# Optimization experiments

Hardware: AMD Instinct MI355X
Metric: run time of the kernel (lower is better)

The kernel has to match this reference:

```python
import jax, jax.numpy as jnp
import numpy as np

B, S, D = 8, 1024, 1024
H, DK, DV = 16, 64, 64
LN_EPS = 1e-5
NEG = -1.0e9


def setup_inputs() -> dict:
    key = jax.random.key(0)
    k1, k2, k3, k4, k5, k6, k7 = jax.random.split(key, 7)
    sc = 0.02
    input_Q = jax.random.normal(k1, (B, S, D), dtype=jnp.float32)
    input_K = jax.random.normal(k2, (B, S, D), dtype=jnp.float32)
    input_V = jax.random.normal(k3, (B, S, D), dtype=jnp.float32)
    # causal mask: True = masked (as in torch masked_fill_)
    attn_mask = jnp.broadcast_to(jnp.triu(jnp.ones((S, S), dtype=bool), k=1), (B, S, S))
    Wq = jax.random.normal(k4, (D, H * DK), dtype=jnp.float32) * sc
    Wk = jax.random.normal(k5, (D, H * DK), dtype=jnp.float32) * sc
    Wv = jax.random.normal(k6, (D, H * DV), dtype=jnp.float32) * sc
    Wfc = jax.random.normal(k7, (H * DV, D), dtype=jnp.float32) * sc
    return {"input_Q": input_Q, "input_K": input_K, "input_V": input_V,
            "attn_mask": attn_mask, "Wq": Wq, "Wk": Wk, "Wv": Wv, "Wfc": Wfc}


def _layernorm(x):
    mu = jnp.mean(x, axis=-1, keepdims=True)
    var = jnp.var(x, axis=-1, keepdims=True)
    return (x - mu) * jax.lax.rsqrt(var + LN_EPS)  # gamma=1, beta=0 (fresh nn.LayerNorm)


def reference(input_Q, input_K, input_V, attn_mask, Wq, Wk, Wv, Wfc):
    residual = input_Q
    # project and split heads: [B,S,H*dk] -> [B,H,S,dk]
    Q = (input_Q @ Wq).reshape(B, S, H, DK).transpose(0, 2, 1, 3)
    K = (input_K @ Wk).reshape(B, S, H, DK).transpose(0, 2, 1, 3)
    V = (input_V @ Wv).reshape(B, S, H, DV).transpose(0, 2, 1, 3)
    scores = jnp.einsum('bhqd,bhkd->bhqk', Q, K) / np.sqrt(DK).astype(np.float32)
    scores = jnp.where(attn_mask[:, None, :, :], NEG, scores)
    attn = jax.nn.softmax(scores, axis=-1)            # [B,H,S,S]
    context = jnp.einsum('bhqk,bhkd->bhqd', attn, V)  # [B,H,S,dv]
    context = context.transpose(0, 2, 1, 3).reshape(B, S, H * DV)
    out = _layernorm(residual + context @ Wfc)        # [B,S,D]
    return out, attn
```

## Files before the change

kernel.cpp:

```cpp
#include <hip/hip_runtime.h>
#include <hip/hip_bf16.h>

#define BB 8
#define SS 1024
#define DD 1024
#define HH 16
#define DKK 64
#define MM (BB*SS)
#define OUT_ELEMS ((size_t)BB*SS*DD)
#define ATTN_ELEMS ((size_t)BB*HH*SS*SS)

using short8 = __attribute__((ext_vector_type(8))) short;
using f32x4  = __attribute__((ext_vector_type(4))) float;

__device__ __forceinline__ ushort f2b(float f) {
    unsigned u = __float_as_uint(f);
    u = u + 0x7fffu + ((u >> 16) & 1u);
    return (ushort)(u >> 16);
}

__global__ __launch_bounds__(256) void transpose_w(
    const float* __restrict__ w0, const float* __restrict__ w1,
    const float* __restrict__ w2, const float* __restrict__ w3,
    ushort* __restrict__ t0, ushort* __restrict__ t1,
    ushort* __restrict__ t2, ushort* __restrict__ t3)
{
    const float* W; ushort* T;
    switch (blockIdx.z) {
        case 0: W = w0; T = t0; break;
        case 1: W = w1; T = t1; break;
        case 2: W = w2; T = t2; break;
        default: W = w3; T = t3; break;
    }
    __shared__ float tile[64 * 65];
    const int k0 = blockIdx.x * 64, n0 = blockIdx.y * 64;
    const int t = threadIdx.x;
#pragma unroll
    for (int i = 0; i < 16; i++) {
        int idx = i * 256 + t;
        int r = idx >> 6, c = idx & 63;
        tile[r * 65 + c] = W[(size_t)(k0 + r) * DD + n0 + c];
    }
    __syncthreads();
#pragma unroll
    for (int i = 0; i < 16; i++) {
        int idx = i * 256 + t;
        int nr = idx >> 6, kc = idx & 63;
        T[(size_t)(n0 + nr) * DD + k0 + kc] = f2b(tile[kc * 65 + nr]);
    }
}

template <int MODE>
__global__ __launch_bounds__(256) void gemm_bt(
    const float* __restrict__ A, const ushort* __restrict__ Bt,
    void* __restrict__ Cout)
{
    constexpr int K = 1024;
    const int t = threadIdx.x;
    const int wg = blockIdx.x;
    const int l  = (wg & 7) * 64 + (wg >> 3);
    const int n0 = (l & 7) * 128, m0 = (l >> 3) * 128;
    const int lane = t & 63, w = t >> 6;
    const int li = lane & 15, quad = lane >> 4;
    const int wm = w >> 1, wn = w & 1;

    __shared__ ushort As[128 * 40];

    f32x4 acc[4][4];
    const f32x4 zf = {0.f, 0.f, 0.f, 0.f};
#pragma unroll
    for (int mf = 0; mf < 4; mf++)
#pragma unroll
        for (int nf = 0; nf < 4; nf++) acc[mf][nf] = zf;

    for (int kk = 0; kk < K; kk += 32) {
        __syncthreads();
#pragma unroll
        for (int i = 0; i < 4; i++) {
            int row = (t >> 3) + i * 32;
            float4 a4 = *(const float4*)&A[(size_t)(m0 + row) * K + kk + (t & 7) * 4];
            ushort4 u4 = make_ushort4(f2b(a4.x), f2b(a4.y), f2b(a4.z), f2b(a4.w));
            *(ushort4*)&As[row * 40 + (t & 7) * 4] = u4;
        }
        __syncthreads();

        short8 af[4], bf[4];
#pragma unroll
        for (int mf = 0; mf < 4; mf++)
            af[mf] = *(const short8*)&As[(wm * 64 + mf * 16 + li) * 40 + quad * 8];
#pragma unroll
        for (int nf = 0; nf < 4; nf++)
            bf[nf] = *(const short8*)&Bt[(size_t)(n0 + wn * 64 + nf * 16 + li) * K + kk + quad * 8];
#pragma unroll
        for (int mf = 0; mf < 4; mf++)
#pragma unroll
            for (int nf = 0; nf < 4; nf++)
                acc[mf][nf] = __builtin_amdgcn_mfma_f32_16x16x32_bf16(af[mf], bf[nf], acc[mf][nf], 0, 0, 0);
    }

#pragma unroll
    for (int mf = 0; mf < 4; mf++)
#pragma unroll
        for (int nf = 0; nf < 4; nf++)
#pragma unroll
            for (int r = 0; r < 4; r++) {
                int m = m0 + wm * 64 + mf * 16 + quad * 4 + r;
                int n = n0 + wn * 64 + nf * 16 + li;
                float v = acc[mf][nf][r];
                if (MODE == 0) {
                    int b = m >> 10, s = m & 1023, h = n >> 6, d = n & 63;
                    ((ushort*)Cout)[((size_t)(b * HH + h) * SS + s) * 64 + d] = f2b(v);
                } else if (MODE == 1) {
                    int b = m >> 10, s = m & 1023, h = n >> 6, d = n & 63;
                    ((ushort*)Cout)[((size_t)(b * HH + h) * 64 + d) * SS + s] = f2b(v);
                } else {
                    ((float*)Cout)[(size_t)m * 1024 + n] = v;
                }
            }
}

__global__ __launch_bounds__(256) void attn_pv(
    const ushort* __restrict__ Qp, const ushort* __restrict__ Kp,
    const ushort* __restrict__ VpT, float* __restrict__ Invs,
    float* __restrict__ Ctx)
{
    const int pr = blockIdx.x;
    const int h  = blockIdx.y;
    const int b  = blockIdx.z;
    const int bh = b * HH + h;
    const int t = threadIdx.x;
    const int w = t >> 6, lane = t & 63;
    const int li = lane & 15, quad = lane >> 4;

    const ushort* Qh = Qp  + (size_t)bh * SS * 64;
    const ushort* Kh = Kp  + (size_t)bh * SS * 64;
    const ushort* Vt = VpT + (size_t)bh * 64 * SS;

    __shared__ ushort Ps[4][16 * 32];
    ushort* myP = Ps[w];
    const f32x4 zf = {0.f, 0.f, 0.f, 0.f};

    for (int sel = 0; sel < 2; sel++) {
        const int qt = sel ? (15 - pr) : pr;
        const int qbase = qt * 64 + w * 16;

        short8 aq0 = *(const short8*)&Qh[(size_t)(qbase + li) * 64 + quad * 8];
        short8 aq1 = *(const short8*)&Qh[(size_t)(qbase + li) * 64 + 32 + quad * 8];

        float lsum[4] = {0.f, 0.f, 0.f, 0.f};
        f32x4 cacc[4];
#pragma unroll
        for (int vf = 0; vf < 4; vf++) cacc[vf] = zf;

        const int nch = (qt + 1) * 2;

        for (int c = 0; c < nch; c++) {
            const int kb = c * 32;
#pragma unroll
            for (int half = 0; half < 2; half++) {
                const int col = kb + half * 16 + li;
                short8 bk0 = *(const short8*)&Kh[(size_t)col * 64 + quad * 8];
                short8 bk1 = *(const short8*)&Kh[(size_t)col * 64 + 32 + quad * 8];
                f32x4 s = __builtin_amdgcn_mfma_f32_16x16x32_bf16(aq0, bk0, zf, 0, 0, 0);
                s = __builtin_amdgcn_mfma_f32_16x16x32_bf16(aq1, bk1, s, 0, 0, 0);
#pragma unroll
                for (int r = 0; r < 4; r++) {
                    const int row = qbase + quad * 4 + r;
                    float p = (col <= row) ? __expf(s[r] * 0.125f) : 0.f;
                    lsum[r] += p;
                    myP[(quad * 4 + r) * 32 + half * 16 + li] = f2b(p);
                }
            }
            asm volatile("" ::: "memory");
            short8 ap = *(const short8*)&myP[li * 32 + quad * 8];
#pragma unroll
            for (int vf = 0; vf < 4; vf++) {
                short8 bv = *(const short8*)&Vt[(size_t)(vf * 16 + li) * SS + kb + quad * 8];
                cacc[vf] = __builtin_amdgcn_mfma_f32_16x16x32_bf16(ap, bv, cacc[vf], 0, 0, 0);
            }
            asm volatile("" ::: "memory");
        }

#pragma unroll
        for (int r = 0; r < 4; r++) {
            float v = lsum[r];
            v += __shfl_xor(v, 1, 64);
            v += __shfl_xor(v, 2, 64);
            v += __shfl_xor(v, 4, 64);
            v += __shfl_xor(v, 8, 64);
            lsum[r] = 1.f / v;
        }
        if (li == 0) {
#pragma unroll
            for (int r = 0; r < 4; r++)
                Invs[(size_t)bh * SS + qbase + quad * 4 + r] = lsum[r];
        }

#pragma unroll
        for (int vf = 0; vf < 4; vf++)
#pragma unroll
            for (int r = 0; r < 4; r++) {
                const int s_idx = qbase + quad * 4 + r;
                Ctx[((size_t)b * SS + s_idx) * DD + h * 64 + vf * 16 + li] = cacc[vf][r] * lsum[r];
            }
    }
}

__global__ __launch_bounds__(256) void attn_write(
    const ushort* __restrict__ Qp, const ushort* __restrict__ Kp,
    const float* __restrict__ Invs, float* __restrict__ attn)
{
    const int qt = blockIdx.x >> 1;
    const int ch = blockIdx.x & 1;
    const int h  = blockIdx.y;
    const int b  = blockIdx.z;
    const int bh = b * HH + h;
    const int t = threadIdx.x;
    const int w = t >> 6, lane = t & 63;
    const int li = lane & 15, quad = lane >> 4;
    const int qbase = qt * 64 + w * 16;
    const int c0 = ch * 512;

    const ushort* Qh = Qp + (size_t)bh * SS * 64;
    const ushort* Kh = Kp + (size_t)bh * SS * 64;
    float* arow = attn + (size_t)bh * SS * SS;

    const f32x4 zf = {0.f, 0.f, 0.f, 0.f};

    short8 aq0 = *(const short8*)&Qh[(size_t)(qbase + li) * 64 + quad * 8];
    short8 aq1 = *(const short8*)&Qh[(size_t)(qbase + li) * 64 + 32 + quad * 8];
    float inv[4];
#pragma unroll
    for (int r = 0; r < 4; r++)
        inv[r] = Invs[(size_t)bh * SS + qbase + quad * 4 + r];

    for (int c64 = 0; c64 < 8; c64++) {
        const int kb = c0 + c64 * 64;
        if (kb > qbase + 15) {
#pragma unroll
            for (int r = 0; r < 4; r++) {
                const int row = qbase + quad * 4 + r;
                *(f32x4*)&arow[(size_t)row * SS + kb + li * 4] = zf;
            }
        } else {
#pragma unroll
            for (int q16 = 0; q16 < 4; q16++) {
                const int col = kb + q16 * 16 + li;
                short8 bk0 = *(const short8*)&Kh[(size_t)col * 64 + quad * 8];
                short8 bk1 = *(const short8*)&Kh[(size_t)col * 64 + 32 + quad * 8];
                f32x4 s = __builtin_amdgcn_mfma_f32_16x16x32_bf16(aq0, bk0, zf, 0, 0, 0);
                s = __builtin_amdgcn_mfma_f32_16x16x32_bf16(aq1, bk1, s, 0, 0, 0);
#pragma unroll
                for (int r = 0; r < 4; r++) {
                    const int row = qbase + quad * 4 + r;
                    float p = (col <= row) ? __expf(s[r] * 0.125f) * inv[r] : 0.f;
                    arow[(size_t)row * SS + col] = p;
                }
            }
        }
    }
}

__global__ __launch_bounds__(256) void ln_kernel(
    const float* __restrict__ res, float* __restrict__ io)
{
    const int row = blockIdx.x;
    const int t = threadIdx.x;
    float4 p4 = *(const float4*)&io[(size_t)row * DD + t * 4];
    float4 r4 = *(const float4*)&res[(size_t)row * DD + t * 4];
    float x0 = p4.x + r4.x, x1 = p4.y + r4.y, x2 = p4.z + r4.z, x3 = p4.w + r4.w;
    float s  = x0 + x1 + x2 + x3;
    float ss = x0 * x0 + x1 * x1 + x2 * x2 + x3 * x3;
#pragma unroll
    for (int m = 1; m < 64; m <<= 1) {
        s  += __shfl_xor(s, m, 64);
        ss += __shfl_xor(ss, m, 64);
    }
    __shared__ float red[8];
    const int w = t >> 6, lane = t & 63;
    if (lane == 0) { red[w] = s; red[4 + w] = ss; }
    __syncthreads();
    if (t == 0) {
        float S1 = red[0] + red[1] + red[2] + red[3];
        float S2 = red[4] + red[5] + red[6] + red[7];
        float mu = S1 * (1.f / 1024.f);
        float var = S2 * (1.f / 1024.f) - mu * mu;
        red[0] = mu;
        red[1] = rsqrtf(var + 1e-5f);
    }
    __syncthreads();
    float mu = red[0], rs = red[1];
    float4 o;
    o.x = (x0 - mu) * rs; o.y = (x1 - mu) * rs;
    o.z = (x2 - mu) * rs; o.w = (x3 - mu) * rs;
    *(float4*)&io[(size_t)row * DD + t * 4] = o;
}

extern "C" void kernel_launch(void* const* d_in, const int* in_sizes, int n_in,
                              void* d_out, int out_size, void* d_ws, size_t ws_size,
                              hipStream_t stream)
{
    const float* Xq  = (const float*)d_in[0];
    const float* Xk  = (const float*)d_in[1];
    const float* Xv  = (const float*)d_in[2];
    const float* Wq  = (const float*)d_in[4];
    const float* Wk  = (const float*)d_in[5];
    const float* Wv  = (const float*)d_in[6];
    const float* Wfc = (const float*)d_in[7];

    char* ws = (char*)d_ws;
    ushort* Wt0 = (ushort*)ws;
    ushort* Wt1 = Wt0 + (size_t)1024 * 1024;
    ushort* Wt2 = Wt1 + (size_t)1024 * 1024;
    ushort* Wt3 = Wt2 + (size_t)1024 * 1024;
    ushort* Qp  = (ushort*)(ws + ((size_t)8  << 20));
    ushort* Kp  = (ushort*)(ws + ((size_t)24 << 20));
    ushort* VpT = (ushort*)(ws + ((size_t)40 << 20));
    float*  Ctx = (float*) (ws + ((size_t)56 << 20));
    float*  Invs = (float*)ws;

    float* outp = (float*)d_out;
    float* attn = outp + OUT_ELEMS;

    transpose_w<<<dim3(16, 16, 4), 256, 0, stream>>>(Wq, Wk, Wv, Wfc, Wt0, Wt1, Wt2, Wt3);
    gemm_bt<0><<<dim3(512), 256, 0, stream>>>(Xq, Wt0, Qp);
    gemm_bt<0><<<dim3(512), 256, 0, stream>>>(Xk, Wt1, Kp);
    gemm_bt<1><<<dim3(512), 256, 0, stream>>>(Xv, Wt2, VpT);
    attn_pv<<<dim3(8, 16, 8), 256, 0, stream>>>(Qp, Kp, VpT, Invs, Ctx);
    attn_write<<<dim3(32, 16, 8), 256, 0, stream>>>(Qp, Kp, Invs, attn);
    gemm_bt<2><<<dim3(512), 256, 0, stream>>>(Ctx, Wt3, outp);
    ln_kernel<<<MM, 256, 0, stream>>>(Xq, outp);
}
```

Measured before the change: 1.158 ms.

## Pre-convert GEMM inputs to bf16, stage A/B via global_load_lds, remap attention grids

Adds a separate fp32-to-bf16 conversion pass for each projection input, and rewrites the GEMM so both A and B tiles are staged into LDS with direct global-to-LDS loads instead of converting A in-kernel and reading B straight from global memory. The attention context is now written as bf16, which halves its traffic and feeds the output GEMM directly. The attention kernels use 1D grids with a remapped block order, intended to spread work across XCDs and improve cache locality. The cost is extra conversion kernels and intermediate traffic, unpadded LDS rows that may cause bank conflicts, and lower precision for the context.

```diff
diff --git a/kernel.cpp b/kernel.cpp
--- a/kernel.cpp
+++ b/kernel.cpp
@@ -10,13 +10,20 @@
 #define OUT_ELEMS ((size_t)BB*SS*DD)
 #define ATTN_ELEMS ((size_t)BB*HH*SS*SS)
 
-using short8 = __attribute__((ext_vector_type(8))) short;
-using f32x4  = __attribute__((ext_vector_type(4))) float;
+using short8  = __attribute__((ext_vector_type(8))) short;
+using ushort8 = __attribute__((ext_vector_type(8))) ushort;
+using f32x4   = __attribute__((ext_vector_type(4))) float;
 
 __device__ __forceinline__ ushort f2b(float f) {
     unsigned u = __float_as_uint(f);
     u = u + 0x7fffu + ((u >> 16) & 1u);
     return (ushort)(u >> 16);
+}
+
+__device__ __forceinline__ void glds16(const ushort* g, ushort* l) {
+    __builtin_amdgcn_global_load_lds(
+        (const __attribute__((address_space(1))) void*)g,
+        (__attribute__((address_space(3))) void*)l, 16, 0, 0);
 }
 
 __global__ __launch_bounds__(256) void transpose_w(
@@ -50,9 +57,21 @@
     }
 }
 
+__global__ __launch_bounds__(256) void convert_bf16(
+    const float* __restrict__ in, ushort* __restrict__ out)
+{
+    const size_t i = ((size_t)blockIdx.x * 256 + threadIdx.x) * 8;
+    float4 a = *(const float4*)&in[i];
+    float4 b = *(const float4*)&in[i + 4];
+    ushort8 o;
+    o[0] = f2b(a.x); o[1] = f2b(a.y); o[2] = f2b(a.z); o[3] = f2b(a.w);
+    o[4] = f2b(b.x); o[5] = f2b(b.y); o[6] = f2b(b.z); o[7] = f2b(b.w);
+    *(ushort8*)&out[i] = o;
+}
+
 template <int MODE>
-__global__ __launch_bounds__(256) void gemm_bt(
-    const float* __restrict__ A, const ushort* __restrict__ Bt,
+__global__ __launch_bounds__(256) void gemm_a16(
+    const ushort* __restrict__ Ab, const ushort* __restrict__ Bt,
     void* __restrict__ Cout)
 {
     constexpr int K = 1024;
@@ -64,7 +83,20 @@
     const int li = lane & 15, quad = lane >> 4;
     const int wm = w >> 1, wn = w & 1;
 
-    __shared__ ushort As[128 * 40];
+    __shared__ ushort As[128 * 32];
+    __shared__ ushort Bs[128 * 32];
+
+    const int srow0 = w * 16 + (lane >> 2);
+    const int srow1 = (w + 4) * 16 + (lane >> 2);
+    const int scol  = (lane & 3) * 8;
+    const ushort* gA0 = &Ab[(size_t)(m0 + srow0) * K + scol];
+    const ushort* gA1 = &Ab[(size_t)(m0 + srow1) * K + scol];
+    const ushort* gB0 = &Bt[(size_t)(n0 + srow0) * K + scol];
+    const ushort* gB1 = &Bt[(size_t)(n0 + srow1) * K + scol];
+    ushort* lA0 = &As[(size_t)w * 512];
+    ushort* lA1 = &As[(size_t)(w + 4) * 512];
+    ushort* lB0 = &Bs[(size_t)w * 512];
+    ushort* lB1 = &Bs[(size_t)(w + 4) * 512];
 
     f32x4 acc[4][4];
     const f32x4 zf = {0.f, 0.f, 0.f, 0.f};
@@ -75,27 +107,24 @@
 
     for (int kk = 0; kk < K; kk += 32) {
         __syncthreads();
-#pragma unroll
-        for (int i = 0; i < 4; i++) {
-            int row = (t >> 3) + i * 32;
-            float4 a4 = *(const float4*)&A[(size_t)(m0 + row) * K + kk + (t & 7) * 4];
-            ushort4 u4 = make_ushort4(f2b(a4.x), f2b(a4.y), f2b(a4.z), f2b(a4.w));
-            *(ushort4*)&As[row * 40 + (t & 7) * 4] = u4;
-        }
+        glds16(gA0 + kk, lA0);
+        glds16(gA1 + kk, lA1);
+        glds16(gB0 + kk, lB0);
+        glds16(gB1 + kk, lB1);
         __syncthreads();
 
-        short8 af[4], bf[4];
+        short8 af[4], bfr[4];
 #pragma unroll
         for (int mf = 0; mf < 4; mf++)
-            af[mf] = *(const short8*)&As[(wm * 64 + mf * 16 + li) * 40 + quad * 8];
+            af[mf] = *(const short8*)&As[(wm * 64 + mf * 16 + li) * 32 + quad * 8];
 #pragma unroll
         for (int nf = 0; nf < 4; nf++)
-            bf[nf] = *(const short8*)&Bt[(size_t)(n0 + wn * 64 + nf * 16 + li) * K + kk + quad * 8];
+            bfr[nf] = *(const short8*)&Bs[(wn * 64 + nf * 16 + li) * 32 + quad * 8];
 #pragma unroll
         for (int mf = 0; mf < 4; mf++)
 #pragma unroll
             for (int nf = 0; nf < 4; nf++)
-                acc[mf][nf] = __builtin_amdgcn_mfma_f32_16x16x32_bf16(af[mf], bf[nf], acc[mf][nf], 0, 0, 0);
+                acc[mf][nf] = __builtin_amdgcn_mfma_f32_16x16x32_bf16(af[mf], bfr[nf], acc[mf][nf], 0, 0, 0);
     }
 
 #pragma unroll
@@ -122,12 +151,13 @@
 __global__ __launch_bounds__(256) void attn_pv(
     const ushort* __restrict__ Qp, const ushort* __restrict__ Kp,
     const ushort* __restrict__ VpT, float* __restrict__ Invs,
-    float* __restrict__ Ctx)
-{
-    const int pr = blockIdx.x;
-    const int h  = blockIdx.y;
-    const int b  = blockIdx.z;
-    const int bh = b * HH + h;
+    ushort* __restrict__ CtxB)
+{
+    const int wg = blockIdx.x;
+    const int lid = (wg & 7) * 128 + (wg >> 3);
+    const int pr = lid & 7;
+    const int bh = lid >> 3;
+    const int h = bh & 15, b = bh >> 4;
     const int t = threadIdx.x;
     const int w = t >> 6, lane = t & 63;
     const int li = lane & 15, quad = lane >> 4;
@@ -201,7 +231,7 @@
 #pragma unroll
             for (int r = 0; r < 4; r++) {
                 const int s_idx = qbase + quad * 4 + r;
-                Ctx[((size_t)b * SS + s_idx) * DD + h * 64 + vf * 16 + li] = cacc[vf][r] * lsum[r];
+                CtxB[((size_t)b * SS + s_idx) * DD + h * 64 + vf * 16 + li] = f2b(cacc[vf][r] * lsum[r]);
             }
     }
 }
@@ -210,11 +240,11 @@
     const ushort* __restrict__ Qp, const ushort* __restrict__ Kp,
     const float* __restrict__ Invs, float* __restrict__ attn)
 {
-    const int qt = blockIdx.x >> 1;
-    const int ch = blockIdx.x & 1;
-    const int h  = blockIdx.y;
-    const int b  = blockIdx.z;
-    const int bh = b * HH + h;
+    const int wg = blockIdx.x;
+    const int lid = (wg & 7) * 512 + (wg >> 3);
+    const int bh = lid >> 5;
+    const int qt = (lid & 31) >> 1;
+    const int ch = lid & 1;
     const int t = threadIdx.x;
     const int w = t >> 6, lane = t & 63;
     const int li = lane & 15, quad = lane >> 4;
@@ -316,18 +346,21 @@
     ushort* Qp  = (ushort*)(ws + ((size_t)8  << 20));
     ushort* Kp  = (ushort*)(ws + ((size_t)24 << 20));
     ushort* VpT = (ushort*)(ws + ((size_t)40 << 20));
-    float*  Ctx = (float*) (ws + ((size_t)56 << 20));
+    ushort* Xb  = (ushort*)(ws + ((size_t)56 << 20));
     float*  Invs = (float*)ws;
 
     float* outp = (float*)d_out;
     float* attn = outp + OUT_ELEMS;
 
     transpose_w<<<dim3(16, 16, 4), 256, 0, stream>>>(Wq, Wk, Wv, Wfc, Wt0, Wt1, Wt2, Wt3);
-    gemm_bt<0><<<dim3(512), 256, 0, stream>>>(Xq, Wt0, Qp);
-    gemm_bt<0><<<dim3(512), 256, 0, stream>>>(Xk, Wt1, Kp);
-    gemm_bt<1><<<dim3(512), 256, 0, stream>>>(Xv, Wt2, VpT);
-    attn_pv<<<dim3(8, 16, 8), 256, 0, stream>>>(Qp, Kp, VpT, Invs, Ctx);
-    attn_write<<<dim3(32, 16, 8), 256, 0, stream>>>(Qp, Kp, Invs, attn);
-    gemm_bt<2><<<dim3(512), 256, 0, stream>>>(Ctx, Wt3, outp);
+    convert_bf16<<<4096, 256, 0, stream>>>(Xq, Xb);
+    gemm_a16<0><<<512, 256, 0, stream>>>(Xb, Wt0, Qp);
+    convert_bf16<<<4096, 256, 0, stream>>>(Xk, Xb);
+    gemm_a16<0><<<512, 256, 0, stream>>>(Xb, Wt1, Kp);
+    convert_bf16<<<4096, 256, 0, stream>>>(Xv, Xb);
+    gemm_a16<1><<<512, 256, 0, stream>>>(Xb, Wt2, VpT);
+    attn_pv<<<1024, 256, 0, stream>>>(Qp, Kp, VpT, Invs, Xb);
+    attn_write<<<4096, 256, 0, stream>>>(Qp, Kp, Invs, attn);
+    gemm_a16<2><<<512, 256, 0, stream>>>(Xb, Wt3, outp);
     ln_kernel<<<MM, 256, 0, stream>>>(Xq, outp);
 }
```

Result: faster. 990.8 us (-14.4%).
